# Optimization experiments

Measured on AMD Instinct MI355X. Metric: run time of the kernel, lower is better.

Reference implementation:

```python
import jax, jax.numpy as jnp
import numpy as np

N_FEATURES = 128
N_ACTIONS = 16
HIDDEN = 256
BATCH = 4096
IN_DIM = N_FEATURES + N_ACTIONS  # 144


def setup_inputs() -> dict:
    key = jax.random.key(0)
    k1, k2, k3, k4 = jax.random.split(key, 4)
    f_t = jax.random.normal(k1, (BATCH, N_FEATURES), dtype=jnp.float32)
    a_t = jax.random.normal(k2, (BATCH, N_ACTIONS), dtype=jnp.float32)
    # Stacked per-feature MLP params (one small MLP per output feature).
    W1 = jax.random.normal(k3, (N_FEATURES, IN_DIM, HIDDEN), dtype=jnp.float32) / np.sqrt(IN_DIM)
    b1 = jnp.zeros((N_FEATURES, HIDDEN), dtype=jnp.float32)
    W2 = jax.random.normal(k4, (N_FEATURES, HIDDEN), dtype=jnp.float32) / np.sqrt(HIDDEN)
    b2 = jnp.zeros((N_FEATURES,), dtype=jnp.float32)
    return {"f_t": f_t, "a_t": a_t, "W1": W1, "b1": b1, "W2": W2, "b2": b2}


def reference(f_t, a_t, W1, b1, W2, b2):
    # fa_t: [B, F+A] shared input to all per-feature models
    fa_t = jnp.concatenate((f_t, a_t), axis=1)
    # Grouped GEMM replacing parallel_apply over n_features tiny MLPs:
    # h: [M, B, H]
    h = jax.nn.relu(jnp.einsum('bi,mih->mbh', fa_t, W1) + b1[:, None, :])
    # out: [B, M]  (each model emits a single scalar per example)
    out = jnp.einsum('mbh,mh->bm', h, W2) + b2[None, :]
    # skip_connection=True, additional=False, all=False -> add f_t
    return out + f_t
```

## Files before the change

kernel.cpp:

```cpp
#include <hip/hip_runtime.h>
#include <hip/hip_bf16.h>

#define BATCH   4096
#define NF      128
#define NA      16
#define IN_DIM  144
#define KP      160
#define KF      192
#define HID     256

typedef __attribute__((ext_vector_type(8))) short bf16x8;
typedef __attribute__((ext_vector_type(4))) float f32x4;
typedef unsigned int u32;

__device__ __forceinline__ void gl_lds16(const void* gsrc, void* ldst) {
    __builtin_amdgcn_global_load_lds(
        (const __attribute__((address_space(1))) u32*)gsrc,
        (__attribute__((address_space(3))) u32*)ldst, 16, 0, 0);
}

__global__ void convert_all(const float* __restrict__ W1,
                            const float* __restrict__ b1,
                            const float* __restrict__ f_t,
                            const float* __restrict__ a_t,
                            __hip_bfloat16* __restrict__ w1t,
                            __hip_bfloat16* __restrict__ fab) {
    const int bid = blockIdx.x;
    const int t = threadIdx.x;
    if (bid < 1280) {
        __shared__ float tile[16][HID];
        int m = bid / 10;
        int kc = bid - m * 10;
        int k0 = kc * 16;
        if (kc < 9) {
#pragma unroll
            for (int i = 0; i < 16; ++i)
                tile[i][t] = W1[((size_t)m * IN_DIM + (k0 + i)) * HID + t];
            __syncthreads();
            union { ushort us[16]; uint4 q[2]; } pk;
#pragma unroll
            for (int i = 0; i < 16; ++i) {
                __hip_bfloat16 h = __float2bfloat16(tile[i][t]);
                pk.us[i] = *(ushort*)&h;
            }
            uint4* dst = (uint4*)(w1t + ((size_t)m * HID + t) * KP + k0);
            dst[0] = pk.q[0];
            dst[1] = pk.q[1];
        } else {
            union { ushort us[8]; uint4 q; } pk;
#pragma unroll
            for (int j = 0; j < 8; ++j) pk.us[j] = 0;
            __hip_bfloat16 hb = __float2bfloat16(b1[(size_t)m * HID + t]);
            pk.us[0] = *(ushort*)&hb;
            uint4 z = {0u, 0u, 0u, 0u};
            uint4* dst = (uint4*)(w1t + ((size_t)m * HID + t) * KP + IN_DIM);
            dst[0] = pk.q;
            dst[1] = z;
        }
    } else {
        int c = (bid - 1280) * 256 + t;
        const int total = BATCH * (KF / 8);
        if (c >= total) return;
        int row = c / 24;
        int cc = c - row * 24;
        union { ushort us[8]; uint4 q; } pk;
#pragma unroll
        for (int j = 0; j < 8; ++j) {
            int k = cc * 8 + j;
            float v;
            if (k < NF)            v = f_t[(size_t)row * NF + k];
            else if (k < IN_DIM)   v = a_t[(size_t)row * NA + (k - NF)];
            else if (k == IN_DIM)  v = 1.0f;
            else                   v = 0.0f;
            __hip_bfloat16 h = __float2bfloat16(v);
            pk.us[j] = *(ushort*)&h;
        }
        int pc = cc ^ (row & 7);
        *(uint4*)(fab + (size_t)row * KF + pc * 8) = pk.q;
    }
}

__global__ __launch_bounds__(256) void fused_mlp(
        const __hip_bfloat16* __restrict__ fab,
        const __hip_bfloat16* __restrict__ w1t,
        const float* __restrict__ W2,
        const float* __restrict__ b2,
        const float* __restrict__ f_t,
        float* __restrict__ out) {
    __shared__ __align__(16) __hip_bfloat16 Abuf[2][64 * KF];
    __shared__ __align__(16) float partial[2][4][64];

    const int bid = blockIdx.x;
    const int m     = bid & 127;
    const int slice = bid >> 7;
    const int row_base = slice * 512;
    const int t = threadIdx.x;
    const int w = t >> 6;
    const int lane = t & 63;
    const int lrow = lane & 15;
    const int g = lane >> 4;
    const int xr = (lrow & 7) << 4;

    bf16x8 bfrag[4][5];
#pragma unroll
    for (int hi = 0; hi < 4; ++hi) {
        const int col = w * 64 + hi * 16 + lrow;
        const __hip_bfloat16* wp = w1t + ((size_t)m * HID + col) * KP + g * 8;
#pragma unroll
        for (int ks = 0; ks < 5; ++ks)
            bfrag[hi][ks] = *(const bf16x8*)(wp + ks * 32);
    }
    f32x4 w2v[4];
#pragma unroll
    for (int hi = 0; hi < 4; ++hi)
        w2v[hi] = *(const f32x4*)(W2 + (size_t)m * HID + w * 64 + hi * 16 + g * 4);
    const float b2v = b2[m];

    {
        const char* src = (const char*)(fab + (size_t)row_base * KF);
        char* dst = (char*)&Abuf[0][0];
#pragma unroll
        for (int i = 0; i < 6; ++i)
            gl_lds16(src + (size_t)(t + i * 256) * 16, dst + (t + i * 256) * 16);
    }
    __syncthreads();

    for (int tile = 0; tile < 8; ++tile) {
        const int cur = tile & 1;
        const int r0 = row_base + tile * 64;

        if (tile < 7) {
            const char* src = (const char*)(fab + (size_t)(r0 + 64) * KF);
            char* dst = (char*)&Abuf[cur ^ 1][0];
#pragma unroll
            for (int i = 0; i < 6; ++i)
                gl_lds16(src + (size_t)(t + i * 256) * 16, dst + (t + i * 256) * 16);
        }
        float skipv = 0.0f;
        if (t < 64) skipv = f_t[(size_t)(r0 + t) * NF + m];

        f32x4 acc[4][4];
#pragma unroll
        for (int hi = 0; hi < 4; ++hi)
#pragma unroll
            for (int bj = 0; bj < 4; ++bj)
                acc[hi][bj] = (f32x4){0.f, 0.f, 0.f, 0.f};

        const char* ab = (const char*)&Abuf[cur][0];
#pragma unroll
        for (int ks = 0; ks < 5; ++ks) {
            bf16x8 a[4];
#pragma unroll
            for (int bj = 0; bj < 4; ++bj) {
                int off = (bj * 16 + lrow) * 384 + ((ks * 64 + g * 16) ^ xr);
                a[bj] = *(const bf16x8*)(ab + off);
            }
#pragma unroll
            for (int hi = 0; hi < 4; ++hi)
#pragma unroll
                for (int bj = 0; bj < 4; ++bj)
                    acc[hi][bj] = __builtin_amdgcn_mfma_f32_16x16x32_bf16(
                        bfrag[hi][ks], a[bj], acc[hi][bj], 0, 0, 0);
        }

        float sarr[4];
#pragma unroll
        for (int bj = 0; bj < 4; ++bj) {
            float sr0 = 0.f, sr1 = 0.f, sr2 = 0.f, sr3 = 0.f;
#pragma unroll
            for (int hi = 0; hi < 4; ++hi) {
                float h0 = acc[hi][bj][0]; h0 = h0 > 0.f ? h0 : 0.f;
                float h1 = acc[hi][bj][1]; h1 = h1 > 0.f ? h1 : 0.f;
                float h2 = acc[hi][bj][2]; h2 = h2 > 0.f ? h2 : 0.f;
                float h3 = acc[hi][bj][3]; h3 = h3 > 0.f ? h3 : 0.f;
                sr0 = fmaf(h0, w2v[hi][0], sr0);
                sr1 = fmaf(h1, w2v[hi][1], sr1);
                sr2 = fmaf(h2, w2v[hi][2], sr2);
                sr3 = fmaf(h3, w2v[hi][3], sr3);
            }
            float s = (sr0 + sr1) + (sr2 + sr3);
            s += __shfl_xor(s, 16, 64);
            s += __shfl_xor(s, 32, 64);
            sarr[bj] = s;
        }
        float sv = (g == 0) ? sarr[0] : (g == 1) ? sarr[1]
                 : (g == 2) ? sarr[2] : sarr[3];
        partial[cur][w][lane] = sv;

        __syncthreads();
        if (t < 64) {
            float v = partial[cur][0][t] + partial[cur][1][t]
                    + partial[cur][2][t] + partial[cur][3][t]
                    + b2v + skipv;
            out[(size_t)(r0 + t) * NF + m] = v;
        }
    }
}

extern "C" void kernel_launch(void* const* d_in, const int* in_sizes, int n_in,
                              void* d_out, int out_size, void* d_ws, size_t ws_size,
                              hipStream_t stream) {
    const float* f_t = (const float*)d_in[0];
    const float* a_t = (const float*)d_in[1];
    const float* W1  = (const float*)d_in[2];
    const float* b1  = (const float*)d_in[3];
    const float* W2  = (const float*)d_in[4];
    const float* b2  = (const float*)d_in[5];
    float* out = (float*)d_out;

    __hip_bfloat16* w1t = (__hip_bfloat16*)d_ws;
    __hip_bfloat16* fab = (__hip_bfloat16*)((char*)d_ws + (size_t)NF * HID * KP * 2);

    hipLaunchKernelGGL(convert_all, dim3(1664), dim3(256), 0, stream,
                       W1, b1, f_t, a_t, w1t, fab);
    hipLaunchKernelGGL(fused_mlp, dim3(1024), dim3(256), 0, stream,
                       fab, w1t, W2, b2, f_t, out);
}
```

Baseline: 60.58 us.

## Switch to 32x32x16 MFMA and double rows per block

Replaces the 16x16x32 bf16 MFMA tiling with 32x32x16 MFMA instructions. This reduces LDS A-fragment loads per K step and shrinks the cross-lane reduction to a single shuffle. Each block now processes 1024 rows over 16 tiles with half as many blocks, amortising the per-block W1 fragment loads. The trade-off is 512 blocks on a 256-CU device, which lowers parallelism, plus a launch_bounds occupancy hint.

```diff
diff --git a/kernel.cpp b/kernel.cpp
--- a/kernel.cpp
+++ b/kernel.cpp
@@ -11,6 +11,7 @@
 
 typedef __attribute__((ext_vector_type(8))) short bf16x8;
 typedef __attribute__((ext_vector_type(4))) float f32x4;
+typedef __attribute__((ext_vector_type(16))) float f32x16;
 typedef unsigned int u32;
 
 __device__ __forceinline__ void gl_lds16(const void* gsrc, void* ldst) {
@@ -80,7 +81,7 @@
     }
 }
 
-__global__ __launch_bounds__(256) void fused_mlp(
+__global__ __launch_bounds__(256, 2) void fused_mlp(
         const __hip_bfloat16* __restrict__ fab,
         const __hip_bfloat16* __restrict__ w1t,
         const float* __restrict__ W2,
@@ -93,28 +94,39 @@
     const int bid = blockIdx.x;
     const int m     = bid & 127;
     const int slice = bid >> 7;
-    const int row_base = slice * 512;
+    const int row_base = slice * 1024;
     const int t = threadIdx.x;
     const int w = t >> 6;
     const int lane = t & 63;
-    const int lrow = lane & 15;
-    const int g = lane >> 4;
-    const int xr = (lrow & 7) << 4;
-
-    bf16x8 bfrag[4][5];
-#pragma unroll
-    for (int hi = 0; hi < 4; ++hi) {
-        const int col = w * 64 + hi * 16 + lrow;
-        const __hip_bfloat16* wp = w1t + ((size_t)m * HID + col) * KP + g * 8;
-#pragma unroll
-        for (int ks = 0; ks < 5; ++ks)
-            bfrag[hi][ks] = *(const bf16x8*)(wp + ks * 32);
-    }
-    f32x4 w2v[4];
-#pragma unroll
-    for (int hi = 0; hi < 4; ++hi)
-        w2v[hi] = *(const f32x4*)(W2 + (size_t)m * HID + w * 64 + hi * 16 + g * 4);
+    const int l31 = lane & 31;
+    const int h = lane >> 5;
+    const int xr = (l31 & 7) << 4;
+
+    bf16x8 bfrag[2][10];
+#pragma unroll
+    for (int hi2 = 0; hi2 < 2; ++hi2) {
+        const int col = w * 64 + hi2 * 32 + l31;
+        const __hip_bfloat16* wp = w1t + ((size_t)m * HID + col) * KP + h * 8;
+#pragma unroll
+        for (int ks = 0; ks < 10; ++ks)
+            bfrag[hi2][ks] = *(const bf16x8*)(wp + ks * 16);
+    }
+    f32x16 w2v[2];
+#pragma unroll
+    for (int hi2 = 0; hi2 < 2; ++hi2) {
+        const float* wp2 = W2 + (size_t)m * HID + w * 64 + hi2 * 32 + 4 * h;
+#pragma unroll
+        for (int q = 0; q < 4; ++q) {
+            f32x4 v = *(const f32x4*)(wp2 + 8 * q);
+            w2v[hi2][q * 4 + 0] = v[0];
+            w2v[hi2][q * 4 + 1] = v[1];
+            w2v[hi2][q * 4 + 2] = v[2];
+            w2v[hi2][q * 4 + 3] = v[3];
+        }
+    }
     const float b2v = b2[m];
+    const f32x16 zc = (f32x16){0.f,0.f,0.f,0.f,0.f,0.f,0.f,0.f,
+                               0.f,0.f,0.f,0.f,0.f,0.f,0.f,0.f};
 
     {
         const char* src = (const char*)(fab + (size_t)row_base * KF);
@@ -125,11 +137,11 @@
     }
     __syncthreads();
 
-    for (int tile = 0; tile < 8; ++tile) {
+    for (int tile = 0; tile < 16; ++tile) {
         const int cur = tile & 1;
         const int r0 = row_base + tile * 64;
 
-        if (tile < 7) {
+        if (tile < 15) {
             const char* src = (const char*)(fab + (size_t)(r0 + 64) * KF);
             char* dst = (char*)&Abuf[cur ^ 1][0];
 #pragma unroll
@@ -139,58 +151,71 @@
         float skipv = 0.0f;
         if (t < 64) skipv = f_t[(size_t)(r0 + t) * NF + m];
 
-        f32x4 acc[4][4];
-#pragma unroll
-        for (int hi = 0; hi < 4; ++hi)
-#pragma unroll
-            for (int bj = 0; bj < 4; ++bj)
-                acc[hi][bj] = (f32x4){0.f, 0.f, 0.f, 0.f};
-
+        f32x16 acc[2][2];
         const char* ab = (const char*)&Abuf[cur][0];
-#pragma unroll
-        for (int ks = 0; ks < 5; ++ks) {
-            bf16x8 a[4];
-#pragma unroll
-            for (int bj = 0; bj < 4; ++bj) {
-                int off = (bj * 16 + lrow) * 384 + ((ks * 64 + g * 16) ^ xr);
-                a[bj] = *(const bf16x8*)(ab + off);
+
+        {
+            bf16x8 a[2];
+#pragma unroll
+            for (int bj2 = 0; bj2 < 2; ++bj2) {
+                int row = bj2 * 32 + l31;
+                int off = row * 384 + ((h * 16) ^ xr);
+                a[bj2] = *(const bf16x8*)(ab + off);
             }
 #pragma unroll
-            for (int hi = 0; hi < 4; ++hi)
-#pragma unroll
-                for (int bj = 0; bj < 4; ++bj)
-                    acc[hi][bj] = __builtin_amdgcn_mfma_f32_16x16x32_bf16(
-                        bfrag[hi][ks], a[bj], acc[hi][bj], 0, 0, 0);
-        }
-
-        float sarr[4];
-#pragma unroll
-        for (int bj = 0; bj < 4; ++bj) {
+            for (int hi2 = 0; hi2 < 2; ++hi2)
+#pragma unroll
+                for (int bj2 = 0; bj2 < 2; ++bj2)
+                    acc[hi2][bj2] = __builtin_amdgcn_mfma_f32_32x32x16_bf16(
+                        bfrag[hi2][0], a[bj2], zc, 0, 0, 0);
+        }
+#pragma unroll
+        for (int ks = 1; ks < 10; ++ks) {
+            bf16x8 a[2];
+#pragma unroll
+            for (int bj2 = 0; bj2 < 2; ++bj2) {
+                int row = bj2 * 32 + l31;
+                int off = row * 384 + ((ks * 32 + h * 16) ^ xr);
+                a[bj2] = *(const bf16x8*)(ab + off);
+            }
+#pragma unroll
+            for (int hi2 = 0; hi2 < 2; ++hi2)
+#pragma unroll
+                for (int bj2 = 0; bj2 < 2; ++bj2)
+                    acc[hi2][bj2] = __builtin_amdgcn_mfma_f32_32x32x16_bf16(
+                        bfrag[hi2][ks], a[bj2], acc[hi2][bj2], 0, 0, 0);
+        }
+
+        float sarr[2];
+#pragma unroll
+        for (int bj2 = 0; bj2 < 2; ++bj2) {
             float sr0 = 0.f, sr1 = 0.f, sr2 = 0.f, sr3 = 0.f;
 #pragma unroll
-            for (int hi = 0; hi < 4; ++hi) {
-                float h0 = acc[hi][bj][0]; h0 = h0 > 0.f ? h0 : 0.f;
-                float h1 = acc[hi][bj][1]; h1 = h1 > 0.f ? h1 : 0.f;
-                float h2 = acc[hi][bj][2]; h2 = h2 > 0.f ? h2 : 0.f;
-                float h3 = acc[hi][bj][3]; h3 = h3 > 0.f ? h3 : 0.f;
-                sr0 = fmaf(h0, w2v[hi][0], sr0);
-                sr1 = fmaf(h1, w2v[hi][1], sr1);
-                sr2 = fmaf(h2, w2v[hi][2], sr2);
-                sr3 = fmaf(h3, w2v[hi][3], sr3);
-            }
+            for (int hi2 = 0; hi2 < 2; ++hi2)
+#pragma unroll
+                for (int q = 0; q < 4; ++q) {
+                    float h0 = acc[hi2][bj2][q*4+0]; h0 = h0 > 0.f ? h0 : 0.f;
+                    float h1 = acc[hi2][bj2][q*4+1]; h1 = h1 > 0.f ? h1 : 0.f;
+                    float h2 = acc[hi2][bj2][q*4+2]; h2 = h2 > 0.f ? h2 : 0.f;
+                    float h3 = acc[hi2][bj2][q*4+3]; h3 = h3 > 0.f ? h3 : 0.f;
+                    sr0 = fmaf(h0, w2v[hi2][q*4+0], sr0);
+                    sr1 = fmaf(h1, w2v[hi2][q*4+1], sr1);
+                    sr2 = fmaf(h2, w2v[hi2][q*4+2], sr2);
+                    sr3 = fmaf(h3, w2v[hi2][q*4+3], sr3);
+                }
             float s = (sr0 + sr1) + (sr2 + sr3);
-            s += __shfl_xor(s, 16, 64);
             s += __shfl_xor(s, 32, 64);
-            sarr[bj] = s;
-        }
-        float sv = (g == 0) ? sarr[0] : (g == 1) ? sarr[1]
-                 : (g == 2) ? sarr[2] : sarr[3];
-        partial[cur][w][lane] = sv;
+            sarr[bj2] = s;
+        }
+        if (h == 0) {
+            partial[cur][w][l31]      = sarr[0];
+            partial[cur][w][32 + l31] = sarr[1];
+        }
 
         __syncthreads();
         if (t < 64) {
-            float v = partial[cur][0][t] + partial[cur][1][t]
-                    + partial[cur][2][t] + partial[cur][3][t]
+            float v = (partial[cur][0][t] + partial[cur][1][t])
+                    + (partial[cur][2][t] + partial[cur][3][t])
                     + b2v + skipv;
             out[(size_t)(r0 + t) * NF + m] = v;
         }
@@ -213,6 +238,6 @@
 
     hipLaunchKernelGGL(convert_all, dim3(1664), dim3(256), 0, stream,
                        W1, b1, f_t, a_t, w1t, fab);
-    hipLaunchKernelGGL(fused_mlp, dim3(1024), dim3(256), 0, stream,
+    hipLaunchKernelGGL(fused_mlp, dim3(512), dim3(256), 0, stream,
                        fab, w1t, W2, b2, f_t, out);
 }
```

Measured after the change: 58.83 us. 1.03x faster.
